# Optimization experiments

Hardware: AMD Instinct MI355X
Metric: run time of the kernel (lower is better)

The kernel has to match this reference:

```python
import jax, jax.numpy as jnp
import numpy as np

HIDDEN = 450
DEPTH = 4
ATOM_FDIM = 35
BOND_FDIM = 5
MAX_NB = 15
N_ATOMS = 30000
N_BONDS = 60000
N_MESS = 10001
N_MOLS = 1000
EPS = 1e-5


def setup_inputs() -> dict:
    key = jax.random.key(0)
    ks = jax.random.split(key, 10)
    fatoms = jax.random.normal(ks[0], (N_ATOMS, ATOM_FDIM), dtype=jnp.float32)
    fbonds = jax.random.normal(ks[1], (N_BONDS, ATOM_FDIM + BOND_FDIM), dtype=jnp.float32)
    # indices into concatenated [tree_message; graph_message] table (index 0 = zero pad slot)
    agraph = jax.random.randint(ks[2], (N_ATOMS, MAX_NB), 0, N_MESS + N_BONDS)
    bgraph = jax.random.randint(ks[3], (N_BONDS, MAX_NB), 0, N_MESS + N_BONDS)
    per_mol = N_ATOMS // N_MOLS
    starts = jnp.arange(N_MOLS, dtype=jnp.int64) * per_mol
    lens = jnp.full((N_MOLS,), per_mol, dtype=jnp.int64)
    scope = jnp.stack([starts, lens], axis=1)
    tree_message = jax.random.normal(ks[4], (N_MESS, HIDDEN), dtype=jnp.float32)
    tree_message = tree_message.at[0].set(0.0)  # padding row
    s = 0.05
    W_i = jax.random.normal(ks[5], (HIDDEN, ATOM_FDIM + BOND_FDIM), dtype=jnp.float32) * s
    W_h = jax.random.normal(ks[6], (HIDDEN, HIDDEN), dtype=jnp.float32) * s
    W_o = jax.random.normal(ks[7], (HIDDEN, ATOM_FDIM + HIDDEN), dtype=jnp.float32) * s
    b_o = jax.random.normal(ks[8], (HIDDEN,), dtype=jnp.float32) * s
    gamma = jnp.ones((HIDDEN,), dtype=jnp.float32)
    beta = jnp.zeros((HIDDEN,), dtype=jnp.float32)
    return {"fatoms": fatoms, "fbonds": fbonds, "agraph": agraph, "bgraph": bgraph,
            "scope": scope, "tree_message": tree_message, "W_i": W_i, "W_h": W_h,
            "W_o": W_o, "b_o": b_o, "gamma": gamma, "beta": beta}


def reference(fatoms, fbonds, agraph, bgraph, scope, tree_message, W_i, W_h, W_o, b_o, gamma, beta):
    # bond input features -> hidden
    binput = fbonds @ W_i.T                      # [n_bonds, H]
    graph_message = jax.nn.relu(binput)
    # message-passing loop (dropout is identity in eval / p=0)
    for _ in range(DEPTH - 1):
        message = jnp.concatenate([tree_message, graph_message], axis=0)
        nei = message[bgraph].sum(axis=1)        # padded-neighbor gather + sum -> [n_bonds, H]
        graph_message = jax.nn.relu(binput + nei @ W_h.T)
    message = jnp.concatenate([tree_message, graph_message], axis=0)
    nei = message[agraph].sum(axis=1)            # [n_atoms, H]
    ainput = jnp.concatenate([fatoms, nei], axis=1)
    h = ainput @ W_o.T + b_o                     # [n_atoms, H]
    # BatchNorm1d (training-mode batch statistics, biased variance)
    mean = h.mean(axis=0)
    var = ((h - mean) ** 2).mean(axis=0)
    h = (h - mean) * jax.lax.rsqrt(var + EPS) * gamma + beta
    h = jax.nn.relu(h)
    # scope-based segment mean pooling
    starts = scope[:, 0]
    lens = scope[:, 1]
    mol_id = jnp.searchsorted(starts, jnp.arange(N_ATOMS), side="right") - 1
    sums = jax.ops.segment_sum(h, mol_id, num_segments=N_MOLS)
    denom = jnp.maximum(lens, 1).astype(h.dtype)[:, None]
    return jnp.where(lens[:, None] > 0, sums / denom, jnp.zeros_like(sums))
```

## Files before the change

### kernel.cpp

```cpp
#include <hip/hip_runtime.h>
#include <cstdint>
#include <cstddef>

#define HIDDEN 450
#define ATOM_FDIM 35
#define IN_FDIM 40
#define MAX_NB 15
#define N_ATOMS 30000
#define N_BONDS 60000
#define N_MESS 10001
#define N_MOLS 1000
#define DEPTH 4
#define NTOT (N_MESS + N_BONDS)

#define KPAD 512
#define MB_PAD 60032
#define MA_PAD 30080

typedef _Float16 f16x8_t __attribute__((ext_vector_type(8)));
typedef float f32x4_t __attribute__((ext_vector_type(4)));
typedef unsigned short ushort8_t __attribute__((ext_vector_type(8)));

__device__ __forceinline__ float h2f(unsigned short u) {
    return (float)__builtin_bit_cast(_Float16, u);
}
__device__ __forceinline__ unsigned short f2h(float f) {
    return __builtin_bit_cast(unsigned short, (_Float16)f);
}
__device__ __forceinline__ void st_out(unsigned short* p, float v) { *p = f2h(v); }
__device__ __forceinline__ void st_out(float* p, float v) { *p = v; }

__device__ __forceinline__ void g2l16(const unsigned short* g, unsigned short* l) {
    __builtin_amdgcn_global_load_lds(
        (const __attribute__((address_space(1))) void*)g,
        (__attribute__((address_space(3))) void*)l, 16, 0, 0);
}

__device__ __forceinline__ bool sniff_is64(const void* g) {
    const int* g32 = (const int*)g;
    return (g32[1] | g32[3] | g32[5] | g32[7]) == 0;
}
__device__ __forceinline__ long long load_idx(const void* g, size_t pos, bool is64) {
    return is64 ? ((const long long*)g)[pos] : (long long)((const int*)g)[pos];
}

__global__ void zero_stats_kernel(float* __restrict__ p) {
    int i = blockIdx.x * blockDim.x + threadIdx.x;
    if (i < 2 * HIDDEN) p[i] = 0.f;
}

__global__ void build_wih_kernel(const float* __restrict__ W_i,
                                 const float* __restrict__ W_h,
                                 unsigned short* __restrict__ Wih) {
    int t = blockIdx.x * blockDim.x + threadIdx.x;
    if (t >= KPAD * KPAD) return;
    int n = t >> 9, k = t & 511;
    float v = 0.f;
    if (n < HIDDEN) {
        if (k < IN_FDIM)            v = W_i[(size_t)n * IN_FDIM + k];
        else if (k < IN_FDIM + HIDDEN) v = W_h[(size_t)n * HIDDEN + (k - IN_FDIM)];
    }
    Wih[t] = f2h(v);
}

__global__ void build_wo_kernel(const float* __restrict__ W_o,
                                unsigned short* __restrict__ Wo) {
    int t = blockIdx.x * blockDim.x + threadIdx.x;
    if (t >= KPAD * KPAD) return;
    int n = t >> 9, k = t & 511;
    float v = 0.f;
    if (n < HIDDEN) {
        if (k < ATOM_FDIM)                   v = W_o[(size_t)n * (ATOM_FDIM + HIDDEN) + k];
        else if (k >= IN_FDIM && k < IN_FDIM + HIDDEN)
            v = W_o[(size_t)n * (ATOM_FDIM + HIDDEN) + ATOM_FDIM + (k - IN_FDIM)];
    }
    Wo[t] = f2h(v);
}

__global__ void cvt_fbonds_kernel(const float* __restrict__ fbonds,
                                  unsigned short* __restrict__ Ab) {
    int t = blockIdx.x * blockDim.x + threadIdx.x;
    if (t >= MB_PAD * 10) return;
    int r = t / 10, c = t % 10;
    int col0 = (c < 8) ? c * 8 : 496 + (c - 8) * 8;
    ushort8_t o;
    #pragma unroll
    for (int j = 0; j < 8; ++j) {
        int cc = col0 + j;
        float v = (r < N_BONDS && cc < IN_FDIM) ? fbonds[(size_t)r * IN_FDIM + cc] : 0.f;
        o[j] = f2h(v);
    }
    *(ushort8_t*)(Ab + (size_t)r * KPAD + col0) = o;
}

__global__ void cvt_fatoms_kernel(const float* __restrict__ fatoms,
                                  unsigned short* __restrict__ Aa) {
    int t = blockIdx.x * blockDim.x + threadIdx.x;
    if (t >= MA_PAD * 7) return;
    int r = t / 7, c = t % 7;
    int col0 = (c < 5) ? c * 8 : 496 + (c - 5) * 8;
    ushort8_t o;
    #pragma unroll
    for (int j = 0; j < 8; ++j) {
        int cc = col0 + j;
        float v = (r < N_ATOMS && cc < ATOM_FDIM) ? fatoms[(size_t)r * ATOM_FDIM + cc] : 0.f;
        o[j] = f2h(v);
    }
    *(ushort8_t*)(Aa + (size_t)r * KPAD + col0) = o;
}

__global__ void cvt_tree_kernel(const float* __restrict__ tree,
                                unsigned short* __restrict__ tb) {
    int t = blockIdx.x * blockDim.x + threadIdx.x;
    if (t >= N_MESS * 64) return;
    int r = t >> 6, c8 = (t & 63) * 8;
    ushort8_t o;
    #pragma unroll
    for (int j = 0; j < 8; ++j) {
        int c = c8 + j;
        float v = (c < HIDDEN) ? tree[(size_t)r * HIDDEN + c] : 0.f;
        o[j] = f2h(v);
    }
    *(ushort8_t*)(tb + (size_t)r * KPAD + c8) = o;
}

__global__ void zero_gmpad_kernel(unsigned short* __restrict__ gm) {
    int t = blockIdx.x * blockDim.x + threadIdx.x;
    if (t >= N_BONDS * 8) return;
    int r = t >> 3, c = 448 + (t & 7) * 8;
    ushort8_t z = {0, 0, 0, 0, 0, 0, 0, 0};
    *(ushort8_t*)(gm + (size_t)r * KPAD + c) = z;
}

template<bool RELU, bool BIAS, typename OT>
__global__ __launch_bounds__(256)
void mfma_gemm_kernel(const unsigned short* __restrict__ A,
                      const unsigned short* __restrict__ B,
                      const float* __restrict__ bias,
                      OT* __restrict__ Out, int ldo,
                      int M, int Nvalid, int K, int mtiles)
{
    __shared__ unsigned short As[128 * 32];
    __shared__ unsigned short Bs[128 * 32];
    const int g = blockIdx.x;
    const int mt = (g >> 5) * 8 + (g & 7);
    const int nt = (g >> 3) & 3;
    if (mt >= mtiles) return;
    const int m0 = mt * 128, n0 = nt * 128;

    const int tid  = threadIdx.x;
    const int wave = tid >> 6, lane = tid & 63;
    const int wm = wave >> 1, wn = wave & 1;

    const unsigned short* At = A + (size_t)m0 * KPAD;
    const unsigned short* Bt = B + (size_t)n0 * KPAD;

    const int c0 = wave * 128 + lane;
    const int c1 = c0 + 64;
    const int rA0 = c0 >> 2, kc0 = (c0 & 3) * 8;
    const int rA1 = c1 >> 2, kc1 = (c1 & 3) * 8;
    unsigned short* lA0 = &As[(size_t)(wave * 128) * 8];
    unsigned short* lA1 = &As[(size_t)(wave * 128 + 64) * 8];
    unsigned short* lB0 = &Bs[(size_t)(wave * 128) * 8];
    unsigned short* lB1 = &Bs[(size_t)(wave * 128 + 64) * 8];

    const int fr = lane & 15, kof = (lane >> 4) * 8;

    f32x4_t acc[4][4];
    #pragma unroll
    for (int mi = 0; mi < 4; ++mi)
        #pragma unroll
        for (int ni = 0; ni < 4; ++ni)
            acc[mi][ni] = f32x4_t{0.f, 0.f, 0.f, 0.f};

    for (int k0 = 0; k0 < K; k0 += 32) {
        g2l16(At + (size_t)rA0 * KPAD + k0 + kc0, lA0);
        g2l16(At + (size_t)rA1 * KPAD + k0 + kc1, lA1);
        g2l16(Bt + (size_t)rA0 * KPAD + k0 + kc0, lB0);
        g2l16(Bt + (size_t)rA1 * KPAD + k0 + kc1, lB1);
        __syncthreads();

        f16x8_t a[4], b[4];
        #pragma unroll
        for (int mi = 0; mi < 4; ++mi)
            a[mi] = __builtin_bit_cast(f16x8_t,
                *(const ushort8_t*)&As[(size_t)((wm * 64 + mi * 16 + fr) * 32 + kof)]);
        #pragma unroll
        for (int ni = 0; ni < 4; ++ni)
            b[ni] = __builtin_bit_cast(f16x8_t,
                *(const ushort8_t*)&Bs[(size_t)((wn * 64 + ni * 16 + fr) * 32 + kof)]);
        #pragma unroll
        for (int mi = 0; mi < 4; ++mi)
            #pragma unroll
            for (int ni = 0; ni < 4; ++ni)
                acc[mi][ni] = __builtin_amdgcn_mfma_f32_16x16x32_f16(
                    a[mi], b[ni], acc[mi][ni], 0, 0, 0);
        __syncthreads();
    }

    #pragma unroll
    for (int mi = 0; mi < 4; ++mi) {
        int row_b = m0 + wm * 64 + mi * 16 + (lane >> 4) * 4;
        #pragma unroll
        for (int ni = 0; ni < 4; ++ni) {
            int col = n0 + wn * 64 + ni * 16 + fr;
            if (col >= Nvalid) continue;
            float bi = BIAS ? bias[col] : 0.f;
            #pragma unroll
            for (int r = 0; r < 4; ++r) {
                int row = row_b + r;
                if (row >= M) continue;
                float v = acc[mi][ni][r] + bi;
                if (RELU) v = fmaxf(v, 0.f);
                st_out(&Out[(size_t)row * ldo + col], v);
            }
        }
    }
}

__global__ __launch_bounds__(256)
void gather_kernel(const void* __restrict__ graph, int n_rows,
                   const unsigned short* __restrict__ tree,
                   const unsigned short* __restrict__ gm,
                   unsigned short* __restrict__ Adst)
{
    const bool is64 = sniff_is64(graph);
    int w    = (int)((blockIdx.x * 256 + threadIdx.x) >> 6);
    int lane = threadIdx.x & 63;
    if (w >= n_rows) return;
    const size_t coff = (size_t)lane * 8;

    const unsigned short* rp[MAX_NB];
    #pragma unroll
    for (int nb = 0; nb < MAX_NB; ++nb) {
        long long idx = load_idx(graph, (size_t)w * MAX_NB + nb, is64);
        if (idx < 0) idx = 0;
        if (idx >= NTOT) idx = NTOT - 1;
        int i32 = __builtin_amdgcn_readfirstlane((int)idx);
        rp[nb] = (i32 < N_MESS) ? tree + (size_t)i32 * KPAD
                                : gm + (size_t)(i32 - N_MESS) * KPAD;
    }
    ushort8_t v[MAX_NB];
    #pragma unroll
    for (int nb = 0; nb < MAX_NB; ++nb)
        v[nb] = *(const ushort8_t*)(rp[nb] + coff);

    float acc[8] = {};
    #pragma unroll
    for (int nb = 0; nb < MAX_NB; ++nb)
        #pragma unroll
        for (int j = 0; j < 8; ++j)
            acc[j] += h2f(v[nb][j]);

    if (lane < 57) {
        ushort8_t o;
        #pragma unroll
        for (int j = 0; j < 8; ++j) o[j] = f2h(acc[j]);
        *(ushort8_t*)(Adst + (size_t)w * KPAD + IN_FDIM + coff) = o;
    }
}

__global__ __launch_bounds__(256)
void colstats_kernel(const unsigned short* __restrict__ h,
                     float* __restrict__ sums, float* __restrict__ sumsq)
{
    int t = threadIdx.x;
    int r0 = blockIdx.x * 250;
    float s0 = 0.f, q0 = 0.f, s1 = 0.f, q1 = 0.f;
    bool has1 = t < HIDDEN - 256;
    for (int r = r0; r < r0 + 250; ++r) {
        const unsigned short* row = h + (size_t)r * HIDDEN;
        float v0 = h2f(row[t]);
        s0 += v0; q0 += v0 * v0;
        if (has1) {
            float v1 = h2f(row[t + 256]);
            s1 += v1; q1 += v1 * v1;
        }
    }
    atomicAdd(&sums[t], s0);
    atomicAdd(&sumsq[t], q0);
    if (has1) {
        atomicAdd(&sums[t + 256], s1);
        atomicAdd(&sumsq[t + 256], q1);
    }
}

__global__ void finalize_stats_kernel(const float* __restrict__ sums,
                                      const float* __restrict__ sumsq,
                                      const float* __restrict__ gamma,
                                      const float* __restrict__ beta,
                                      float* __restrict__ scale,
                                      float* __restrict__ shift)
{
    int c = blockIdx.x * blockDim.x + threadIdx.x;
    if (c >= HIDDEN) return;
    float mean = sums[c] * (1.f / N_ATOMS);
    float var  = sumsq[c] * (1.f / N_ATOMS) - mean * mean;
    float inv  = rsqrtf(var + 1e-5f);
    float sc   = gamma[c] * inv;
    scale[c] = sc;
    shift[c] = beta[c] - mean * sc;
}

__global__ __launch_bounds__(256)
void pool_kernel(const unsigned short* __restrict__ h, const void* __restrict__ scope,
                 const float* __restrict__ scale, const float* __restrict__ shift,
                 float* __restrict__ out)
{
    int m = blockIdx.x;
    const int* s32 = (const int*)scope;
    bool is64 = (s32[1] == 0 && s32[3] == 0);
    long long start, len, nxt;
    if (is64) {
        const long long* s = (const long long*)scope;
        start = s[2 * m]; len = s[2 * m + 1];
        nxt = (m < N_MOLS - 1) ? s[2 * m + 2] : (long long)N_ATOMS;
    } else {
        start = s32[2 * m]; len = s32[2 * m + 1];
        nxt = (m < N_MOLS - 1) ? (long long)s32[2 * m + 2] : (long long)N_ATOMS;
    }
    if (start < 0) start = 0;
    if (nxt > N_ATOMS) nxt = N_ATOMS;

    int t = threadIdx.x;
    bool has1 = t < HIDDEN - 256;
    float sc0 = scale[t], sh0 = shift[t];
    float sc1 = 0.f, sh1 = 0.f;
    if (has1) { sc1 = scale[t + 256]; sh1 = shift[t + 256]; }
    float a0 = 0.f, a1 = 0.f;
    for (long long r = start; r < nxt; ++r) {
        const unsigned short* row = h + (size_t)r * HIDDEN;
        a0 += fmaxf(fmaf(h2f(row[t]), sc0, sh0), 0.f);
        if (has1) a1 += fmaxf(fmaf(h2f(row[t + 256]), sc1, sh1), 0.f);
    }
    float den = (float)(len > 0 ? len : 1);
    out[(size_t)m * HIDDEN + t] = (len > 0) ? a0 / den : 0.f;
    if (has1) out[(size_t)m * HIDDEN + t + 256] = (len > 0) ? a1 / den : 0.f;
}

extern "C" void kernel_launch(void* const* d_in, const int* in_sizes, int n_in,
                              void* d_out, int out_size, void* d_ws, size_t ws_size,
                              hipStream_t stream)
{
    const float* fatoms = (const float*)d_in[0];
    const float* fbonds = (const float*)d_in[1];
    const void*  agraph = d_in[2];
    const void*  bgraph = d_in[3];
    const void*  scope  = d_in[4];
    const float* tree   = (const float*)d_in[5];
    const float* W_i    = (const float*)d_in[6];
    const float* W_h    = (const float*)d_in[7];
    const float* W_o    = (const float*)d_in[8];
    const float* b_o    = (const float*)d_in[9];
    const float* gamma  = (const float*)d_in[10];
    const float* beta   = (const float*)d_in[11];
    float* out = (float*)d_out;

    char* ws = (char*)d_ws;
    size_t off = 0;
    auto alloc = [&](size_t bytes) { char* p = ws + off; off += (bytes + 255) & ~(size_t)255; return p; };
    float*          sums  = (float*)alloc(4 * HIDDEN * sizeof(float));
    float*          sumsq = sums + HIDDEN;
    float*          scale = sums + 2 * HIDDEN;
    float*          shift = sums + 3 * HIDDEN;
    unsigned short* Abond = (unsigned short*)alloc((size_t)MB_PAD * KPAD * 2);
    unsigned short* Aatom = (unsigned short*)alloc((size_t)MA_PAD * KPAD * 2);
    unsigned short* gm    = (unsigned short*)alloc((size_t)N_BONDS * KPAD * 2);
    unsigned short* tb    = (unsigned short*)alloc((size_t)N_MESS * KPAD * 2);
    unsigned short* Wih   = (unsigned short*)alloc((size_t)KPAD * KPAD * 2);
    unsigned short* Wo    = (unsigned short*)alloc((size_t)KPAD * KPAD * 2);
    unsigned short* h     = (unsigned short*)alloc((size_t)N_ATOMS * HIDDEN * 2);
    (void)ws_size;

    dim3 blk(256);

    zero_stats_kernel<<<4, blk, 0, stream>>>(sums);
    build_wih_kernel<<<(KPAD * KPAD + 255) / 256, blk, 0, stream>>>(W_i, W_h, Wih);
    build_wo_kernel<<<(KPAD * KPAD + 255) / 256, blk, 0, stream>>>(W_o, Wo);
    cvt_fbonds_kernel<<<(MB_PAD * 10 + 255) / 256, blk, 0, stream>>>(fbonds, Abond);
    cvt_fatoms_kernel<<<(MA_PAD * 7 + 255) / 256, blk, 0, stream>>>(fatoms, Aatom);
    cvt_tree_kernel<<<(N_MESS * 64 + 255) / 256, blk, 0, stream>>>(tree, tb);
    zero_gmpad_kernel<<<(N_BONDS * 8 + 255) / 256, blk, 0, stream>>>(gm);

    dim3 gBond(59 * 32);
    dim3 gAtom(30 * 32);

    mfma_gemm_kernel<true, false, unsigned short><<<gBond, blk, 0, stream>>>(
        Abond, Wih, nullptr, gm, KPAD, N_BONDS, HIDDEN, 64, 469);

    for (int it = 0; it < DEPTH - 1; ++it) {
        gather_kernel<<<N_BONDS / 4, blk, 0, stream>>>(bgraph, N_BONDS, tb, gm, Abond);
        mfma_gemm_kernel<true, false, unsigned short><<<gBond, blk, 0, stream>>>(
            Abond, Wih, nullptr, gm, KPAD, N_BONDS, HIDDEN, KPAD, 469);
    }

    gather_kernel<<<N_ATOMS / 4, blk, 0, stream>>>(agraph, N_ATOMS, tb, gm, Aatom);
    mfma_gemm_kernel<false, true, unsigned short><<<gAtom, blk, 0, stream>>>(
        Aatom, Wo, b_o, h, HIDDEN, N_ATOMS, HIDDEN, KPAD, 235);

    colstats_kernel<<<120, blk, 0, stream>>>(h, sums, sumsq);
    finalize_stats_kernel<<<1, 512, 0, stream>>>(sums, sumsq, gamma, beta, scale, shift);
    pool_kernel<<<N_MOLS, blk, 0, stream>>>(h, scope, scale, shift, out);
}
```

Before: 800.5 us.

## Merge prep kernels, double-buffer GEMM LDS, fuse column stats into epilogue

Merges seven small preprocessing launches into two kernels, one for weights and one grid-stride kernel for data. Double-buffers the GEMM's LDS tiles so the next K-slice's global-to-LDS loads are issued before computing the current one, with one barrier per iteration instead of two. Computes the BatchNorm column sums and sums of squares inside the final atom GEMM epilogue with atomics, which removes the separate colstats pass over h. In exchange, LDS use doubles, and the stats now come from fp32 pre-rounding values and go through many more atomics.

```diff
diff --git a/kernel.cpp b/kernel.cpp
--- a/kernel.cpp
+++ b/kernel.cpp
@@ -44,104 +44,105 @@
     return is64 ? ((const long long*)g)[pos] : (long long)((const int*)g)[pos];
 }
 
-__global__ void zero_stats_kernel(float* __restrict__ p) {
-    int i = blockIdx.x * blockDim.x + threadIdx.x;
-    if (i < 2 * HIDDEN) p[i] = 0.f;
-}
-
-__global__ void build_wih_kernel(const float* __restrict__ W_i,
-                                 const float* __restrict__ W_h,
-                                 unsigned short* __restrict__ Wih) {
+__global__ void prep_w_kernel(const float* __restrict__ W_i,
+                              const float* __restrict__ W_h,
+                              const float* __restrict__ W_o,
+                              unsigned short* __restrict__ Wih,
+                              unsigned short* __restrict__ Wo) {
     int t = blockIdx.x * blockDim.x + threadIdx.x;
-    if (t >= KPAD * KPAD) return;
-    int n = t >> 9, k = t & 511;
-    float v = 0.f;
-    if (n < HIDDEN) {
-        if (k < IN_FDIM)            v = W_i[(size_t)n * IN_FDIM + k];
-        else if (k < IN_FDIM + HIDDEN) v = W_h[(size_t)n * HIDDEN + (k - IN_FDIM)];
-    }
-    Wih[t] = f2h(v);
-}
-
-__global__ void build_wo_kernel(const float* __restrict__ W_o,
-                                unsigned short* __restrict__ Wo) {
-    int t = blockIdx.x * blockDim.x + threadIdx.x;
-    if (t >= KPAD * KPAD) return;
-    int n = t >> 9, k = t & 511;
-    float v = 0.f;
-    if (n < HIDDEN) {
-        if (k < ATOM_FDIM)                   v = W_o[(size_t)n * (ATOM_FDIM + HIDDEN) + k];
-        else if (k >= IN_FDIM && k < IN_FDIM + HIDDEN)
-            v = W_o[(size_t)n * (ATOM_FDIM + HIDDEN) + ATOM_FDIM + (k - IN_FDIM)];
-    }
-    Wo[t] = f2h(v);
-}
-
-__global__ void cvt_fbonds_kernel(const float* __restrict__ fbonds,
-                                  unsigned short* __restrict__ Ab) {
-    int t = blockIdx.x * blockDim.x + threadIdx.x;
-    if (t >= MB_PAD * 10) return;
-    int r = t / 10, c = t % 10;
-    int col0 = (c < 8) ? c * 8 : 496 + (c - 8) * 8;
-    ushort8_t o;
-    #pragma unroll
-    for (int j = 0; j < 8; ++j) {
-        int cc = col0 + j;
-        float v = (r < N_BONDS && cc < IN_FDIM) ? fbonds[(size_t)r * IN_FDIM + cc] : 0.f;
-        o[j] = f2h(v);
-    }
-    *(ushort8_t*)(Ab + (size_t)r * KPAD + col0) = o;
-}
-
-__global__ void cvt_fatoms_kernel(const float* __restrict__ fatoms,
-                                  unsigned short* __restrict__ Aa) {
-    int t = blockIdx.x * blockDim.x + threadIdx.x;
-    if (t >= MA_PAD * 7) return;
-    int r = t / 7, c = t % 7;
-    int col0 = (c < 5) ? c * 8 : 496 + (c - 5) * 8;
-    ushort8_t o;
-    #pragma unroll
-    for (int j = 0; j < 8; ++j) {
-        int cc = col0 + j;
-        float v = (r < N_ATOMS && cc < ATOM_FDIM) ? fatoms[(size_t)r * ATOM_FDIM + cc] : 0.f;
-        o[j] = f2h(v);
-    }
-    *(ushort8_t*)(Aa + (size_t)r * KPAD + col0) = o;
-}
-
-__global__ void cvt_tree_kernel(const float* __restrict__ tree,
-                                unsigned short* __restrict__ tb) {
-    int t = blockIdx.x * blockDim.x + threadIdx.x;
-    if (t >= N_MESS * 64) return;
-    int r = t >> 6, c8 = (t & 63) * 8;
-    ushort8_t o;
-    #pragma unroll
-    for (int j = 0; j < 8; ++j) {
-        int c = c8 + j;
-        float v = (c < HIDDEN) ? tree[(size_t)r * HIDDEN + c] : 0.f;
-        o[j] = f2h(v);
-    }
-    *(ushort8_t*)(tb + (size_t)r * KPAD + c8) = o;
-}
-
-__global__ void zero_gmpad_kernel(unsigned short* __restrict__ gm) {
-    int t = blockIdx.x * blockDim.x + threadIdx.x;
-    if (t >= N_BONDS * 8) return;
-    int r = t >> 3, c = 448 + (t & 7) * 8;
-    ushort8_t z = {0, 0, 0, 0, 0, 0, 0, 0};
-    *(ushort8_t*)(gm + (size_t)r * KPAD + c) = z;
-}
-
-template<bool RELU, bool BIAS, typename OT>
+    if (t < KPAD * KPAD) {
+        int n = t >> 9, k = t & 511;
+        float v = 0.f;
+        if (n < HIDDEN) {
+            if (k < IN_FDIM)               v = W_i[(size_t)n * IN_FDIM + k];
+            else if (k < IN_FDIM + HIDDEN) v = W_h[(size_t)n * HIDDEN + (k - IN_FDIM)];
+        }
+        Wih[t] = f2h(v);
+    } else if (t < 2 * KPAD * KPAD) {
+        int u = t - KPAD * KPAD;
+        int n = u >> 9, k = u & 511;
+        float v = 0.f;
+        if (n < HIDDEN) {
+            if (k < ATOM_FDIM) v = W_o[(size_t)n * (ATOM_FDIM + HIDDEN) + k];
+            else if (k >= IN_FDIM && k < IN_FDIM + HIDDEN)
+                v = W_o[(size_t)n * (ATOM_FDIM + HIDDEN) + ATOM_FDIM + (k - IN_FDIM)];
+        }
+        Wo[u] = f2h(v);
+    }
+}
+
+#define PR_B0 (MB_PAD * 10)
+#define PR_B1 (PR_B0 + MA_PAD * 7)
+#define PR_B2 (PR_B1 + N_MESS * 64)
+#define PR_B3 (PR_B2 + N_BONDS * 8)
+#define PR_B4 (PR_B3 + 1024)
+__global__ void prep_data_kernel(const float* __restrict__ fbonds,
+                                 const float* __restrict__ fatoms,
+                                 const float* __restrict__ tree,
+                                 unsigned short* __restrict__ Ab,
+                                 unsigned short* __restrict__ Aa,
+                                 unsigned short* __restrict__ tb,
+                                 unsigned short* __restrict__ gm,
+                                 float* __restrict__ stats) {
+    for (int t = blockIdx.x * blockDim.x + threadIdx.x; t < PR_B4;
+         t += gridDim.x * blockDim.x) {
+        if (t < PR_B0) {
+            int r = t / 10, c = t % 10;
+            int col0 = (c < 8) ? c * 8 : 496 + (c - 8) * 8;
+            ushort8_t o;
+            #pragma unroll
+            for (int j = 0; j < 8; ++j) {
+                int cc = col0 + j;
+                float v = (r < N_BONDS && cc < IN_FDIM) ? fbonds[(size_t)r * IN_FDIM + cc] : 0.f;
+                o[j] = f2h(v);
+            }
+            *(ushort8_t*)(Ab + (size_t)r * KPAD + col0) = o;
+        } else if (t < PR_B1) {
+            int u = t - PR_B0;
+            int r = u / 7, c = u % 7;
+            int col0 = (c < 5) ? c * 8 : 496 + (c - 5) * 8;
+            ushort8_t o;
+            #pragma unroll
+            for (int j = 0; j < 8; ++j) {
+                int cc = col0 + j;
+                float v = (r < N_ATOMS && cc < ATOM_FDIM) ? fatoms[(size_t)r * ATOM_FDIM + cc] : 0.f;
+                o[j] = f2h(v);
+            }
+            *(ushort8_t*)(Aa + (size_t)r * KPAD + col0) = o;
+        } else if (t < PR_B2) {
+            int u = t - PR_B1;
+            int r = u >> 6, c8 = (u & 63) * 8;
+            ushort8_t o;
+            #pragma unroll
+            for (int j = 0; j < 8; ++j) {
+                int c = c8 + j;
+                float v = (c < HIDDEN) ? tree[(size_t)r * HIDDEN + c] : 0.f;
+                o[j] = f2h(v);
+            }
+            *(ushort8_t*)(tb + (size_t)r * KPAD + c8) = o;
+        } else if (t < PR_B3) {
+            int u = t - PR_B2;
+            int r = u >> 3, c = 448 + (u & 7) * 8;
+            ushort8_t z = {0, 0, 0, 0, 0, 0, 0, 0};
+            *(ushort8_t*)(gm + (size_t)r * KPAD + c) = z;
+        } else {
+            int i = t - PR_B3;
+            if (i < 2 * HIDDEN) stats[i] = 0.f;
+        }
+    }
+}
+
+template<bool RELU, bool BIAS, bool CSTAT, typename OT>
 __global__ __launch_bounds__(256)
 void mfma_gemm_kernel(const unsigned short* __restrict__ A,
                       const unsigned short* __restrict__ B,
                       const float* __restrict__ bias,
                       OT* __restrict__ Out, int ldo,
-                      int M, int Nvalid, int K, int mtiles)
-{
-    __shared__ unsigned short As[128 * 32];
-    __shared__ unsigned short Bs[128 * 32];
+                      int M, int Nvalid, int K, int mtiles,
+                      float* __restrict__ sums, float* __restrict__ sumsq)
+{
+    __shared__ unsigned short As[2][128 * 32];
+    __shared__ unsigned short Bs[2][128 * 32];
     const int g = blockIdx.x;
     const int mt = (g >> 5) * 8 + (g & 7);
     const int nt = (g >> 3) & 3;
@@ -159,10 +160,8 @@
     const int c1 = c0 + 64;
     const int rA0 = c0 >> 2, kc0 = (c0 & 3) * 8;
     const int rA1 = c1 >> 2, kc1 = (c1 & 3) * 8;
-    unsigned short* lA0 = &As[(size_t)(wave * 128) * 8];
-    unsigned short* lA1 = &As[(size_t)(wave * 128 + 64) * 8];
-    unsigned short* lB0 = &Bs[(size_t)(wave * 128) * 8];
-    unsigned short* lB1 = &Bs[(size_t)(wave * 128 + 64) * 8];
+    const int lofs0 = (wave * 128) * 8;
+    const int lofs1 = (wave * 128 + 64) * 8;
 
     const int fr = lane & 15, kof = (lane >> 4) * 8;
 
@@ -173,31 +172,42 @@
         for (int ni = 0; ni < 4; ++ni)
             acc[mi][ni] = f32x4_t{0.f, 0.f, 0.f, 0.f};
 
-    for (int k0 = 0; k0 < K; k0 += 32) {
-        g2l16(At + (size_t)rA0 * KPAD + k0 + kc0, lA0);
-        g2l16(At + (size_t)rA1 * KPAD + k0 + kc1, lA1);
-        g2l16(Bt + (size_t)rA0 * KPAD + k0 + kc0, lB0);
-        g2l16(Bt + (size_t)rA1 * KPAD + k0 + kc1, lB1);
-        __syncthreads();
-
+    auto stage = [&](int buf, int k0) {
+        g2l16(At + (size_t)rA0 * KPAD + k0 + kc0, &As[buf][lofs0]);
+        g2l16(At + (size_t)rA1 * KPAD + k0 + kc1, &As[buf][lofs1]);
+        g2l16(Bt + (size_t)rA0 * KPAD + k0 + kc0, &Bs[buf][lofs0]);
+        g2l16(Bt + (size_t)rA1 * KPAD + k0 + kc1, &Bs[buf][lofs1]);
+    };
+    auto compute = [&](int buf) {
         f16x8_t a[4], b[4];
         #pragma unroll
         for (int mi = 0; mi < 4; ++mi)
             a[mi] = __builtin_bit_cast(f16x8_t,
-                *(const ushort8_t*)&As[(size_t)((wm * 64 + mi * 16 + fr) * 32 + kof)]);
+                *(const ushort8_t*)&As[buf][(size_t)((wm * 64 + mi * 16 + fr) * 32 + kof)]);
         #pragma unroll
         for (int ni = 0; ni < 4; ++ni)
             b[ni] = __builtin_bit_cast(f16x8_t,
-                *(const ushort8_t*)&Bs[(size_t)((wn * 64 + ni * 16 + fr) * 32 + kof)]);
+                *(const ushort8_t*)&Bs[buf][(size_t)((wn * 64 + ni * 16 + fr) * 32 + kof)]);
         #pragma unroll
         for (int mi = 0; mi < 4; ++mi)
             #pragma unroll
             for (int ni = 0; ni < 4; ++ni)
                 acc[mi][ni] = __builtin_amdgcn_mfma_f32_16x16x32_f16(
                     a[mi], b[ni], acc[mi][ni], 0, 0, 0);
+    };
+
+    stage(0, 0);
+    __syncthreads();
+    int cur = 0;
+    for (int k0 = 32; k0 < K; k0 += 32) {
+        stage(cur ^ 1, k0);
+        compute(cur);
         __syncthreads();
-    }
-
+        cur ^= 1;
+    }
+    compute(cur);
+
+    float cs[4] = {0.f, 0.f, 0.f, 0.f}, cq[4] = {0.f, 0.f, 0.f, 0.f};
     #pragma unroll
     for (int mi = 0; mi < 4; ++mi) {
         int row_b = m0 + wm * 64 + mi * 16 + (lane >> 4) * 4;
@@ -211,8 +221,19 @@
                 int row = row_b + r;
                 if (row >= M) continue;
                 float v = acc[mi][ni][r] + bi;
+                if (CSTAT) { cs[ni] += v; cq[ni] += v * v; }
                 if (RELU) v = fmaxf(v, 0.f);
                 st_out(&Out[(size_t)row * ldo + col], v);
+            }
+        }
+    }
+    if (CSTAT) {
+        #pragma unroll
+        for (int ni = 0; ni < 4; ++ni) {
+            int col = n0 + wn * 64 + ni * 16 + fr;
+            if (col < Nvalid) {
+                atomicAdd(&sums[col], cs[ni]);
+                atomicAdd(&sumsq[col], cq[ni]);
             }
         }
     }
@@ -257,31 +278,6 @@
         #pragma unroll
         for (int j = 0; j < 8; ++j) o[j] = f2h(acc[j]);
         *(ushort8_t*)(Adst + (size_t)w * KPAD + IN_FDIM + coff) = o;
-    }
-}
-
-__global__ __launch_bounds__(256)
-void colstats_kernel(const unsigned short* __restrict__ h,
-                     float* __restrict__ sums, float* __restrict__ sumsq)
-{
-    int t = threadIdx.x;
-    int r0 = blockIdx.x * 250;
-    float s0 = 0.f, q0 = 0.f, s1 = 0.f, q1 = 0.f;
-    bool has1 = t < HIDDEN - 256;
-    for (int r = r0; r < r0 + 250; ++r) {
-        const unsigned short* row = h + (size_t)r * HIDDEN;
-        float v0 = h2f(row[t]);
-        s0 += v0; q0 += v0 * v0;
-        if (has1) {
-            float v1 = h2f(row[t + 256]);
-            s1 += v1; q1 += v1 * v1;
-        }
-    }
-    atomicAdd(&sums[t], s0);
-    atomicAdd(&sumsq[t], q0);
-    if (has1) {
-        atomicAdd(&sums[t + 256], s1);
-        atomicAdd(&sumsq[t + 256], q1);
     }
 }
 
@@ -374,31 +370,25 @@
 
     dim3 blk(256);
 
-    zero_stats_kernel<<<4, blk, 0, stream>>>(sums);
-    build_wih_kernel<<<(KPAD * KPAD + 255) / 256, blk, 0, stream>>>(W_i, W_h, Wih);
-    build_wo_kernel<<<(KPAD * KPAD + 255) / 256, blk, 0, stream>>>(W_o, Wo);
-    cvt_fbonds_kernel<<<(MB_PAD * 10 + 255) / 256, blk, 0, stream>>>(fbonds, Abond);
-    cvt_fatoms_kernel<<<(MA_PAD * 7 + 255) / 256, blk, 0, stream>>>(fatoms, Aatom);
-    cvt_tree_kernel<<<(N_MESS * 64 + 255) / 256, blk, 0, stream>>>(tree, tb);
-    zero_gmpad_kernel<<<(N_BONDS * 8 + 255) / 256, blk, 0, stream>>>(gm);
+    prep_w_kernel<<<(2 * KPAD * KPAD + 255) / 256, blk, 0, stream>>>(W_i, W_h, W_o, Wih, Wo);
+    prep_data_kernel<<<2048, blk, 0, stream>>>(fbonds, fatoms, tree, Abond, Aatom, tb, gm, sums);
 
     dim3 gBond(59 * 32);
     dim3 gAtom(30 * 32);
 
-    mfma_gemm_kernel<true, false, unsigned short><<<gBond, blk, 0, stream>>>(
-        Abond, Wih, nullptr, gm, KPAD, N_BONDS, HIDDEN, 64, 469);
+    mfma_gemm_kernel<true, false, false, unsigned short><<<gBond, blk, 0, stream>>>(
+        Abond, Wih, nullptr, gm, KPAD, N_BONDS, HIDDEN, 64, 469, nullptr, nullptr);
 
     for (int it = 0; it < DEPTH - 1; ++it) {
         gather_kernel<<<N_BONDS / 4, blk, 0, stream>>>(bgraph, N_BONDS, tb, gm, Abond);
-        mfma_gemm_kernel<true, false, unsigned short><<<gBond, blk, 0, stream>>>(
-            Abond, Wih, nullptr, gm, KPAD, N_BONDS, HIDDEN, KPAD, 469);
+        mfma_gemm_kernel<true, false, false, unsigned short><<<gBond, blk, 0, stream>>>(
+            Abond, Wih, nullptr, gm, KPAD, N_BONDS, HIDDEN, KPAD, 469, nullptr, nullptr);
     }
 
     gather_kernel<<<N_ATOMS / 4, blk, 0, stream>>>(agraph, N_ATOMS, tb, gm, Aatom);
-    mfma_gemm_kernel<false, true, unsigned short><<<gAtom, blk, 0, stream>>>(
-        Aatom, Wo, b_o, h, HIDDEN, N_ATOMS, HIDDEN, KPAD, 235);
-
-    colstats_kernel<<<120, blk, 0, stream>>>(h, sums, sumsq);
+    mfma_gemm_kernel<false, true, true, unsigned short><<<gAtom, blk, 0, stream>>>(
+        Aatom, Wo, b_o, h, HIDDEN, N_ATOMS, HIDDEN, KPAD, 235, sums, sumsq);
+
     finalize_stats_kernel<<<1, 512, 0, stream>>>(sums, sumsq, gamma, beta, scale, shift);
     pool_kernel<<<N_MOLS, blk, 0, stream>>>(h, scope, scale, shift, out);
 }
```

Result: slower. 908.1 us (+13.4%).
